# Performance work log

Measured on AMD Instinct MI355X. Metric: run time of the kernel, lower is better.

The kernel has to match this reference:

```python
import jax, jax.numpy as jnp
import numpy as np

EPS = 1e-5  # config.layer_norm_epsilon

def setup_inputs() -> dict:
    key = jax.random.key(0)
    ks = jax.random.split(key, 8)
    B, S, D, BOT, N = 8, 2048, 1024, 400, 25
    x = jax.random.normal(ks[0], (B, S, D), dtype=jnp.float32)
    alphas = jax.random.uniform(ks[1], (N,), dtype=jnp.float32) / N
    W_down_all = jax.random.normal(ks[2], (N, BOT, D), dtype=jnp.float32) * 0.02
    W_up_all = jax.random.normal(ks[3], (N, D, BOT), dtype=jnp.float32) * 0.02
    b_down_all = jax.random.normal(ks[4], (N, BOT), dtype=jnp.float32) * 0.02
    b_up_all = jax.random.normal(ks[5], (N, D), dtype=jnp.float32) * 0.02
    W_ln_all = 1.0 + jax.random.normal(ks[6], (N, D), dtype=jnp.float32) * 0.02
    b_ln_all = jax.random.normal(ks[7], (N, D), dtype=jnp.float32) * 0.02
    return {"x": x, "alphas": alphas, "W_down_all": W_down_all, "W_up_all": W_up_all,
            "b_down_all": b_down_all, "b_up_all": b_up_all,
            "W_ln_all": W_ln_all, "b_ln_all": b_ln_all}

def reference(x, alphas, W_down_all, W_up_all, b_down_all, b_up_all, W_ln_all, b_ln_all):
    # Superposition: alpha-weighted sum of all adapters' parameters
    # (original python loop over 25 adapters -> single einsum per tensor).
    W_down = jnp.einsum('n,nbd->bd', alphas, W_down_all)  # [BOT, D]
    W_up   = jnp.einsum('n,ndb->db', alphas, W_up_all)    # [D, BOT]
    W_ln   = jnp.einsum('n,nd->d',  alphas, W_ln_all)     # [D]
    b_ln   = jnp.einsum('n,nd->d',  alphas, b_ln_all)     # [D]
    # b_up / b_down are merged in the original too but passed with bias=None: unused.

    # FAdapter: F.layer_norm with normalized_shape = x.shape[1:], i.e. normalize
    # jointly over (seq, embd) per batch element; ln weight/bias broadcast over seq.
    mu = jnp.mean(x, axis=(1, 2), keepdims=True)
    var = jnp.mean(jnp.square(x - mu), axis=(1, 2), keepdims=True)
    x_ = (x - mu) * jax.lax.rsqrt(var + EPS) * W_ln + b_ln  # [B,S,D]

    h = jax.nn.relu(jnp.einsum('bsd,od->bso', x_, W_down))  # [B,S,BOT], no bias
    x_ = jnp.einsum('bso,do->bsd', h, W_up)                 # [B,S,D],   no bias
    return x + x_
```

## Files before the change

kernel.cpp:

```cpp
#include <hip/hip_runtime.h>
#include <stdint.h>

#define NB   8
#define SS   2048
#define DD   1024
#define BOT  400
#define BOTP 512
#define NAD  25
#define MM   (NB*SS)
#define LN_EPS 1e-5f

typedef __attribute__((ext_vector_type(8))) short bf8_t;
typedef __attribute__((ext_vector_type(4))) float fx4;

__device__ __forceinline__ unsigned short f2bf(float f) {
  unsigned int u = __float_as_uint(f);
  u = (u + 0x7FFFu + ((u >> 16) & 1u)) >> 16;
  return (unsigned short)u;
}

__device__ __forceinline__ void gload16(void* lds, const void* g) {
  __builtin_amdgcn_global_load_lds(
      (const __attribute__((address_space(1))) void*)(uintptr_t)g,
      (__attribute__((address_space(3))) void*)(uint32_t)(uintptr_t)lds,
      16, 0, 0);
}

__global__ __launch_bounds__(256) void mix_kernel(
    const float* __restrict__ alphas,
    const float* __restrict__ WdAll, const float* __restrict__ WuAll,
    const float* __restrict__ wlnAll, const float* __restrict__ blnAll,
    unsigned short* __restrict__ Wd, unsigned short* __restrict__ Wu,
    float* __restrict__ wln, float* __restrict__ bln)
{
  __shared__ float a[NAD];
  const int tid = threadIdx.x;
  if (tid < NAD) a[tid] = alphas[tid];
  __syncthreads();
  const int bid = blockIdx.x;
  if (bid < 512) {
    int g  = bid * 256 + tid;
    int o  = g >> 8;
    int dg = g & 255;
    float4 acc = {0.f, 0.f, 0.f, 0.f};
    if (o < BOT) {
#pragma unroll
      for (int n = 0; n < NAD; ++n) {
        const float4 v = *(const float4*)(WdAll + ((size_t)n * BOT + o) * DD + dg * 4);
        acc.x += a[n] * v.x; acc.y += a[n] * v.y; acc.z += a[n] * v.z; acc.w += a[n] * v.w;
      }
    }
    ushort4 u;
    u.x = f2bf(acc.x); u.y = f2bf(acc.y); u.z = f2bf(acc.z); u.w = f2bf(acc.w);
    *(ushort4*)(Wd + (size_t)o * DD + dg * 4) = u;
  } else if (bid < 1024) {
    int g  = (bid - 512) * 256 + tid;
    int d  = g >> 7;
    int bg = g & 127;
    float4 acc = {0.f, 0.f, 0.f, 0.f};
    if (bg < 100) {
#pragma unroll
      for (int n = 0; n < NAD; ++n) {
        const float4 v = *(const float4*)(WuAll + ((size_t)n * DD + d) * BOT + bg * 4);
        acc.x += a[n] * v.x; acc.y += a[n] * v.y; acc.z += a[n] * v.z; acc.w += a[n] * v.w;
      }
    }
    ushort4 u;
    u.x = f2bf(acc.x); u.y = f2bf(acc.y); u.z = f2bf(acc.z); u.w = f2bf(acc.w);
    *(ushort4*)(Wu + (size_t)d * BOTP + bg * 4) = u;
  } else {
    int i = (bid - 1024) * 256 + tid;
    const float* src = (i < DD) ? wlnAll : blnAll;
    int j = (i < DD) ? i : (i - DD);
    float s = 0.f;
#pragma unroll
    for (int n = 0; n < NAD; ++n) s += a[n] * src[(size_t)n * DD + j];
    if (i < DD) wln[j] = s; else bln[j] = s;
  }
}

__global__ __launch_bounds__(256) void stats_kernel(const float* __restrict__ x,
                                                    float* __restrict__ partials)
{
  const int b = blockIdx.y, c = blockIdx.x;
  const float4* xb = (const float4*)(x + (size_t)b * SS * DD) + (size_t)c * 8192;
  float s = 0.f, q = 0.f;
  for (int i = threadIdx.x; i < 8192; i += 256) {
    float4 v = xb[i];
    s += v.x + v.y + v.z + v.w;
    q += v.x * v.x + v.y * v.y + v.z * v.z + v.w * v.w;
  }
#pragma unroll
  for (int off = 32; off > 0; off >>= 1) { s += __shfl_down(s, off); q += __shfl_down(q, off); }
  __shared__ float red[8];
  const int wave = threadIdx.x >> 6, lane = threadIdx.x & 63;
  if (!lane) { red[wave] = s; red[wave + 4] = q; }
  __syncthreads();
  if (!threadIdx.x) {
    partials[(b * 64 + c) * 2]     = red[0] + red[1] + red[2] + red[3];
    partials[(b * 64 + c) * 2 + 1] = red[4] + red[5] + red[6] + red[7];
  }
}

__global__ __launch_bounds__(256) void norm_kernel(const float* __restrict__ x,
    const float* __restrict__ partials, const float* __restrict__ wln,
    const float* __restrict__ bln, unsigned short* __restrict__ xn)
{
  const int b = blockIdx.y;
  double s = 0.0, q = 0.0;
#pragma unroll 8
  for (int i = 0; i < 64; ++i) {
    s += partials[(b * 64 + i) * 2];
    q += partials[(b * 64 + i) * 2 + 1];
  }
  const double inv = 1.0 / ((double)SS * DD);
  const float mu  = (float)(s * inv);
  const float var = (float)(q * inv) - mu * mu;
  const float rs  = rsqrtf(var + LN_EPS);

  const size_t base = (size_t)b * SS * DD;
  const int idx = blockIdx.x * 256 + threadIdx.x;
  const float4 v  = *(const float4*)(x + base + (size_t)idx * 4);
  const int dg = idx & 255;
  const float4 w  = *(const float4*)(wln + dg * 4);
  const float4 bb = *(const float4*)(bln + dg * 4);
  ushort4 u;
  u.x = f2bf((v.x - mu) * rs * w.x + bb.x);
  u.y = f2bf((v.y - mu) * rs * w.y + bb.y);
  u.z = f2bf((v.z - mu) * rs * w.z + bb.z);
  u.w = f2bf((v.w - mu) * rs * w.w + bb.w);
  *(ushort4*)(xn + base + (size_t)idx * 4) = u;
}

template <int K, bool RELU>
__global__ __launch_bounds__(256) void gemm_bt(
    const unsigned short* __restrict__ A, const unsigned short* __restrict__ Bm,
    const float* __restrict__ Xres, float* __restrict__ Cf,
    unsigned short* __restrict__ Cb, int N)
{
  __shared__ unsigned short As[128 * 32];
  __shared__ unsigned short Bs[128 * 32];
  const int tid  = threadIdx.x;
  const int wave = tid >> 6, lane = tid & 63;
  const int wr = wave >> 1, wc = wave & 1;
  const int nbn  = N >> 7;
  const int bcol = blockIdx.x % nbn, brow = blockIdx.x / nbn;
  const unsigned short* Ab = A + (size_t)brow * 128 * K;
  const unsigned short* Bb = Bm + (size_t)bcol * 128 * K;

  fx4 acc[4][4] = {};

  for (int k0 = 0; k0 < K; k0 += 32) {
#pragma unroll
    for (int i = 0; i < 2; ++i) {
      const int basee = (i * 256 + wave * 64) * 8;
      const int e   = basee + lane * 8;
      const int row = e >> 5, col = e & 31;
      gload16(&As[basee], Ab + (size_t)row * K + k0 + col);
      gload16(&Bs[basee], Bb + (size_t)row * K + k0 + col);
    }
    __syncthreads();

    bf8_t af[4], bf[4];
#pragma unroll
    for (int m = 0; m < 4; ++m)
      af[m] = *(const bf8_t*)&As[(wr * 64 + m * 16 + (lane & 15)) * 32 + (lane >> 4) * 8];
#pragma unroll
    for (int n = 0; n < 4; ++n)
      bf[n] = *(const bf8_t*)&Bs[(wc * 64 + n * 16 + (lane & 15)) * 32 + (lane >> 4) * 8];
#pragma unroll
    for (int m = 0; m < 4; ++m)
#pragma unroll
      for (int n = 0; n < 4; ++n)
        acc[m][n] = __builtin_amdgcn_mfma_f32_16x16x32_bf16(af[m], bf[n], acc[m][n], 0, 0, 0);
    __syncthreads();
  }

  const int r0 = brow * 128 + wr * 64 + ((lane >> 4) << 2);
  const int c0 = bcol * 128 + wc * 64 + (lane & 15);
#pragma unroll
  for (int m = 0; m < 4; ++m) {
#pragma unroll
    for (int n = 0; n < 4; ++n) {
#pragma unroll
      for (int j = 0; j < 4; ++j) {
        const size_t off = (size_t)(r0 + m * 16 + j) * N + (c0 + n * 16);
        float v = acc[m][n][j];
        if (RELU) {
          v = v > 0.f ? v : 0.f;
          Cb[off] = f2bf(v);
        } else {
          Cf[off] = v + Xres[off];
        }
      }
    }
  }
}

extern "C" void kernel_launch(void* const* d_in, const int* in_sizes, int n_in,
                              void* d_out, int out_size, void* d_ws, size_t ws_size,
                              hipStream_t stream)
{
  const float* x      = (const float*)d_in[0];
  const float* alphas = (const float*)d_in[1];
  const float* WdAll  = (const float*)d_in[2];
  const float* WuAll  = (const float*)d_in[3];
  const float* wlnAll = (const float*)d_in[6];
  const float* blnAll = (const float*)d_in[7];
  float* out = (float*)d_out;

  char* ws = (char*)d_ws;
  unsigned short* Wd  = (unsigned short*)ws;
  unsigned short* Wu  = (unsigned short*)(ws + (1u << 20));
  float* wln          = (float*)(ws + (2u << 20));
  float* bln          = wln + DD;
  float* partials     = bln + DD;
  unsigned short* xn  = (unsigned short*)(ws + (3u << 20));
  unsigned short* h   = (unsigned short*)(ws + (35u << 20));

  mix_kernel<<<1032, 256, 0, stream>>>(alphas, WdAll, WuAll, wlnAll, blnAll, Wd, Wu, wln, bln);
  stats_kernel<<<dim3(64, 8), 256, 0, stream>>>(x, partials);
  norm_kernel<<<dim3(2048, 8), 256, 0, stream>>>(x, partials, wln, bln, xn);
  gemm_bt<1024, true ><<<128 * (BOTP / 128), 256, 0, stream>>>(xn, Wd, nullptr, nullptr, h, BOTP);
  gemm_bt<512,  false><<<128 * (DD / 128),   256, 0, stream>>>(h, Wu, x, out, nullptr, DD);
}
```

Baseline: 291.3 us.

## Double-buffer GEMM LDS tiles, swizzle block order, merge mix and stats kernels

Merges the weight-mixing and layer-norm statistics kernels into one launch, so the two independent jobs share a grid and one launch is saved. The GEMM now double-buffers its LDS tiles so the next k-tile loads while MFMAs run on the current one, and the first GEMM uses a 64-wide k-step. Block indices are remapped in an XCD-aware way (blockIdx & 7) to improve L2 locality. The ReLU GEMM stages its bf16 output through LDS to write coalesced 16-byte stores. Doubling the LDS footprint may reduce occupancy.

```diff
diff --git a/kernel.cpp b/kernel.cpp
--- a/kernel.cpp
+++ b/kernel.cpp
@@ -7,7 +7,6 @@
 #define BOT  400
 #define BOTP 512
 #define NAD  25
-#define MM   (NB*SS)
 #define LN_EPS 1e-5f
 
 typedef __attribute__((ext_vector_type(8))) short bf8_t;
@@ -26,18 +25,45 @@
       16, 0, 0);
 }
 
-__global__ __launch_bounds__(256) void mix_kernel(
+__global__ __launch_bounds__(256) void mixstats_kernel(
     const float* __restrict__ alphas,
     const float* __restrict__ WdAll, const float* __restrict__ WuAll,
     const float* __restrict__ wlnAll, const float* __restrict__ blnAll,
+    const float* __restrict__ x,
     unsigned short* __restrict__ Wd, unsigned short* __restrict__ Wu,
-    float* __restrict__ wln, float* __restrict__ bln)
-{
+    float* __restrict__ wln, float* __restrict__ bln,
+    float* __restrict__ partials)
+{
+  const int tid = threadIdx.x;
+  const int bid = blockIdx.x;
+
+  if (bid >= 1032) {
+    const int g = bid - 1032;
+    const int b = g >> 6, c = g & 63;
+    const float4* xb = (const float4*)(x + (size_t)b * SS * DD) + (size_t)c * 8192;
+    float s = 0.f, q = 0.f;
+    for (int i = tid; i < 8192; i += 256) {
+      float4 v = xb[i];
+      s += v.x + v.y + v.z + v.w;
+      q += v.x * v.x + v.y * v.y + v.z * v.z + v.w * v.w;
+    }
+#pragma unroll
+    for (int off = 32; off > 0; off >>= 1) { s += __shfl_down(s, off); q += __shfl_down(q, off); }
+    __shared__ float red[8];
+    const int wave = tid >> 6, lane = tid & 63;
+    if (!lane) { red[wave] = s; red[wave + 4] = q; }
+    __syncthreads();
+    if (!tid) {
+      partials[(b * 64 + c) * 2]     = red[0] + red[1] + red[2] + red[3];
+      partials[(b * 64 + c) * 2 + 1] = red[4] + red[5] + red[6] + red[7];
+    }
+    return;
+  }
+
   __shared__ float a[NAD];
-  const int tid = threadIdx.x;
   if (tid < NAD) a[tid] = alphas[tid];
   __syncthreads();
-  const int bid = blockIdx.x;
+
   if (bid < 512) {
     int g  = bid * 256 + tid;
     int o  = g >> 8;
@@ -76,29 +102,6 @@
 #pragma unroll
     for (int n = 0; n < NAD; ++n) s += a[n] * src[(size_t)n * DD + j];
     if (i < DD) wln[j] = s; else bln[j] = s;
-  }
-}
-
-__global__ __launch_bounds__(256) void stats_kernel(const float* __restrict__ x,
-                                                    float* __restrict__ partials)
-{
-  const int b = blockIdx.y, c = blockIdx.x;
-  const float4* xb = (const float4*)(x + (size_t)b * SS * DD) + (size_t)c * 8192;
-  float s = 0.f, q = 0.f;
-  for (int i = threadIdx.x; i < 8192; i += 256) {
-    float4 v = xb[i];
-    s += v.x + v.y + v.z + v.w;
-    q += v.x * v.x + v.y * v.y + v.z * v.z + v.w * v.w;
-  }
-#pragma unroll
-  for (int off = 32; off > 0; off >>= 1) { s += __shfl_down(s, off); q += __shfl_down(q, off); }
-  __shared__ float red[8];
-  const int wave = threadIdx.x >> 6, lane = threadIdx.x & 63;
-  if (!lane) { red[wave] = s; red[wave + 4] = q; }
-  __syncthreads();
-  if (!threadIdx.x) {
-    partials[(b * 64 + c) * 2]     = red[0] + red[1] + red[2] + red[3];
-    partials[(b * 64 + c) * 2 + 1] = red[4] + red[5] + red[6] + red[7];
   }
 }
 
@@ -132,68 +135,97 @@
   *(ushort4*)(xn + base + (size_t)idx * 4) = u;
 }
 
-template <int K, bool RELU>
+template <int K, int BK, bool RELU>
 __global__ __launch_bounds__(256) void gemm_bt(
     const unsigned short* __restrict__ A, const unsigned short* __restrict__ Bm,
     const float* __restrict__ Xres, float* __restrict__ Cf,
-    unsigned short* __restrict__ Cb, int N)
-{
-  __shared__ unsigned short As[128 * 32];
-  __shared__ unsigned short Bs[128 * 32];
+    unsigned short* __restrict__ Cb, int N, int nbn)
+{
+  __shared__ unsigned short As[2][128 * BK];
+  __shared__ unsigned short Bs[2][128 * BK];
   const int tid  = threadIdx.x;
   const int wave = tid >> 6, lane = tid & 63;
   const int wr = wave >> 1, wc = wave & 1;
-  const int nbn  = N >> 7;
-  const int bcol = blockIdx.x % nbn, brow = blockIdx.x / nbn;
+
+  const int cpx = gridDim.x >> 3;
+  const int bid = (blockIdx.x & 7) * cpx + (blockIdx.x >> 3);
+  const int bcol = bid % nbn, brow = bid / nbn;
   const unsigned short* Ab = A + (size_t)brow * 128 * K;
   const unsigned short* Bb = Bm + (size_t)bcol * 128 * K;
 
-  fx4 acc[4][4] = {};
-
-  for (int k0 = 0; k0 < K; k0 += 32) {
-#pragma unroll
-    for (int i = 0; i < 2; ++i) {
+  constexpr int NL = (128 * BK) / 2048;
+  auto stage = [&](int buf, int k0) {
+#pragma unroll
+    for (int i = 0; i < NL; ++i) {
       const int basee = (i * 256 + wave * 64) * 8;
       const int e   = basee + lane * 8;
-      const int row = e >> 5, col = e & 31;
-      gload16(&As[basee], Ab + (size_t)row * K + k0 + col);
-      gload16(&Bs[basee], Bb + (size_t)row * K + k0 + col);
+      const int row = e / BK, col = e % BK;
+      gload16(&As[buf][basee], Ab + (size_t)row * K + k0 + col);
+      gload16(&Bs[buf][basee], Bb + (size_t)row * K + k0 + col);
+    }
+  };
+
+  fx4 acc[4][4] = {};
+  constexpr int NT = K / BK;
+
+  stage(0, 0);
+  __syncthreads();
+  int cur = 0;
+  for (int t = 0; t < NT; ++t) {
+    if (t + 1 < NT) stage(cur ^ 1, (t + 1) * BK);
+#pragma unroll
+    for (int kk = 0; kk < BK / 32; ++kk) {
+      bf8_t af[4], bf[4];
+#pragma unroll
+      for (int m = 0; m < 4; ++m)
+        af[m] = *(const bf8_t*)&As[cur][(wr * 64 + m * 16 + (lane & 15)) * BK + kk * 32 + (lane >> 4) * 8];
+#pragma unroll
+      for (int n = 0; n < 4; ++n)
+        bf[n] = *(const bf8_t*)&Bs[cur][(wc * 64 + n * 16 + (lane & 15)) * BK + kk * 32 + (lane >> 4) * 8];
+#pragma unroll
+      for (int m = 0; m < 4; ++m)
+#pragma unroll
+        for (int n = 0; n < 4; ++n)
+          acc[m][n] = __builtin_amdgcn_mfma_f32_16x16x32_bf16(af[m], bf[n], acc[m][n], 0, 0, 0);
     }
     __syncthreads();
-
-    bf8_t af[4], bf[4];
+    cur ^= 1;
+  }
+
+  if constexpr (RELU) {
+    unsigned short* Hs = (unsigned short*)As;
+    const int r0l = wr * 64 + ((lane >> 4) << 2);
+    const int c0l = wc * 64 + (lane & 15);
 #pragma unroll
     for (int m = 0; m < 4; ++m)
-      af[m] = *(const bf8_t*)&As[(wr * 64 + m * 16 + (lane & 15)) * 32 + (lane >> 4) * 8];
-#pragma unroll
-    for (int n = 0; n < 4; ++n)
-      bf[n] = *(const bf8_t*)&Bs[(wc * 64 + n * 16 + (lane & 15)) * 32 + (lane >> 4) * 8];
+#pragma unroll
+      for (int n = 0; n < 4; ++n)
+#pragma unroll
+        for (int j = 0; j < 4; ++j) {
+          float v = acc[m][n][j];
+          v = v > 0.f ? v : 0.f;
+          Hs[(r0l + m * 16 + j) * 128 + (c0l + n * 16)] = f2bf(v);
+        }
+    __syncthreads();
+    const size_t outbase = (size_t)(brow * 128) * N + (size_t)bcol * 128;
+#pragma unroll
+    for (int i = 0; i < 8; ++i) {
+      const int idx = i * 256 + tid;
+      const int row = idx >> 4, colg = idx & 15;
+      *(int4*)(Cb + outbase + (size_t)row * N + colg * 8) = *(const int4*)&Hs[row * 128 + colg * 8];
+    }
+  } else {
+    const int r0 = brow * 128 + wr * 64 + ((lane >> 4) << 2);
+    const int c0 = bcol * 128 + wc * 64 + (lane & 15);
 #pragma unroll
     for (int m = 0; m < 4; ++m)
 #pragma unroll
       for (int n = 0; n < 4; ++n)
-        acc[m][n] = __builtin_amdgcn_mfma_f32_16x16x32_bf16(af[m], bf[n], acc[m][n], 0, 0, 0);
-    __syncthreads();
-  }
-
-  const int r0 = brow * 128 + wr * 64 + ((lane >> 4) << 2);
-  const int c0 = bcol * 128 + wc * 64 + (lane & 15);
-#pragma unroll
-  for (int m = 0; m < 4; ++m) {
-#pragma unroll
-    for (int n = 0; n < 4; ++n) {
-#pragma unroll
-      for (int j = 0; j < 4; ++j) {
-        const size_t off = (size_t)(r0 + m * 16 + j) * N + (c0 + n * 16);
-        float v = acc[m][n][j];
-        if (RELU) {
-          v = v > 0.f ? v : 0.f;
-          Cb[off] = f2bf(v);
-        } else {
-          Cf[off] = v + Xres[off];
+#pragma unroll
+        for (int j = 0; j < 4; ++j) {
+          const size_t off = (size_t)(r0 + m * 16 + j) * N + (c0 + n * 16);
+          Cf[off] = acc[m][n][j] + Xres[off];
         }
-      }
-    }
   }
 }
 
@@ -218,9 +250,9 @@
   unsigned short* xn  = (unsigned short*)(ws + (3u << 20));
   unsigned short* h   = (unsigned short*)(ws + (35u << 20));
 
-  mix_kernel<<<1032, 256, 0, stream>>>(alphas, WdAll, WuAll, wlnAll, blnAll, Wd, Wu, wln, bln);
-  stats_kernel<<<dim3(64, 8), 256, 0, stream>>>(x, partials);
+  mixstats_kernel<<<1544, 256, 0, stream>>>(alphas, WdAll, WuAll, wlnAll, blnAll, x,
+                                            Wd, Wu, wln, bln, partials);
   norm_kernel<<<dim3(2048, 8), 256, 0, stream>>>(x, partials, wln, bln, xn);
-  gemm_bt<1024, true ><<<128 * (BOTP / 128), 256, 0, stream>>>(xn, Wd, nullptr, nullptr, h, BOTP);
-  gemm_bt<512,  false><<<128 * (DD / 128),   256, 0, stream>>>(h, Wu, x, out, nullptr, DD);
-}
+  gemm_bt<1024, 64, true ><<<512,  256, 0, stream>>>(xn, Wd, nullptr, nullptr, h, BOTP, BOTP / 128);
+  gemm_bt<512,  32, false><<<1024, 256, 0, stream>>>(h, Wu, x, out, nullptr, DD, DD / 128);
+}
```

Result: slower. 301.5 us (+3.5%).

## Fuse layernorm into first GEMM, double-buffer both GEMMs, rework weight mixing

Applied to the files above, without the earlier changes.

The separate normalize kernel and its bf16 intermediate buffer are removed. The first GEMM now reads fp32 x directly, applies the folded scale and shift while converting to bf16 in LDS, and uses 64-wide K tiles with swizzling and double buffering. The second GEMM also gains double-buffered, swizzled LDS staging. The mix kernel is rewritten with flat indexing, loads hoisted into registers, packed bf16 conversion and explicit zeroing of the padding regions, and the stats kernel uses more chunks. Reading fp32 A costs more bandwidth and registers per tile than reading bf16 A.

```diff
diff --git a/kernel.cpp b/kernel.cpp
--- a/kernel.cpp
+++ b/kernel.cpp
@@ -7,8 +7,8 @@
 #define BOT  400
 #define BOTP 512
 #define NAD  25
-#define MM   (NB*SS)
 #define LN_EPS 1e-5f
+#define NCH  128
 
 typedef __attribute__((ext_vector_type(8))) short bf8_t;
 typedef __attribute__((ext_vector_type(4))) float fx4;
@@ -17,6 +17,11 @@
   unsigned int u = __float_as_uint(f);
   u = (u + 0x7FFFu + ((u >> 16) & 1u)) >> 16;
   return (unsigned short)u;
+}
+__device__ __forceinline__ uint32_t cvtpk(float lo, float hi) {
+  uint32_t r;
+  asm("v_cvt_pk_bf16_f32 %0, %1, %2" : "=v"(r) : "v"(lo), "v"(hi));
+  return r;
 }
 
 __device__ __forceinline__ void gload16(void* lds, const void* g) {
@@ -38,44 +43,46 @@
   if (tid < NAD) a[tid] = alphas[tid];
   __syncthreads();
   const int bid = blockIdx.x;
-  if (bid < 512) {
-    int g  = bid * 256 + tid;
-    int o  = g >> 8;
-    int dg = g & 255;
+
+  if (bid < 800) {
+    const int g = (bid < 400 ? bid : bid - 400) * 256 + tid;
+    const float4* src = (const float4*)(bid < 400 ? WdAll : WuAll) + g;
+    float4 vals[NAD];
+#pragma unroll
+    for (int n = 0; n < NAD; ++n) vals[n] = src[(size_t)n * 102400];
     float4 acc = {0.f, 0.f, 0.f, 0.f};
-    if (o < BOT) {
-#pragma unroll
-      for (int n = 0; n < NAD; ++n) {
-        const float4 v = *(const float4*)(WdAll + ((size_t)n * BOT + o) * DD + dg * 4);
-        acc.x += a[n] * v.x; acc.y += a[n] * v.y; acc.z += a[n] * v.z; acc.w += a[n] * v.w;
-      }
-    }
-    ushort4 u;
-    u.x = f2bf(acc.x); u.y = f2bf(acc.y); u.z = f2bf(acc.z); u.w = f2bf(acc.w);
-    *(ushort4*)(Wd + (size_t)o * DD + dg * 4) = u;
-  } else if (bid < 1024) {
-    int g  = (bid - 512) * 256 + tid;
-    int d  = g >> 7;
-    int bg = g & 127;
-    float4 acc = {0.f, 0.f, 0.f, 0.f};
-    if (bg < 100) {
-#pragma unroll
-      for (int n = 0; n < NAD; ++n) {
-        const float4 v = *(const float4*)(WuAll + ((size_t)n * DD + d) * BOT + bg * 4);
-        acc.x += a[n] * v.x; acc.y += a[n] * v.y; acc.z += a[n] * v.z; acc.w += a[n] * v.w;
-      }
-    }
-    ushort4 u;
-    u.x = f2bf(acc.x); u.y = f2bf(acc.y); u.z = f2bf(acc.z); u.w = f2bf(acc.w);
-    *(ushort4*)(Wu + (size_t)d * BOTP + bg * 4) = u;
+#pragma unroll
+    for (int n = 0; n < NAD; ++n) {
+      acc.x += a[n] * vals[n].x; acc.y += a[n] * vals[n].y;
+      acc.z += a[n] * vals[n].z; acc.w += a[n] * vals[n].w;
+    }
+    uint2 pk = { cvtpk(acc.x, acc.y), cvtpk(acc.z, acc.w) };
+    if (bid < 400) {
+      *(uint2*)(Wd + (size_t)g * 4) = pk;
+    } else {
+      const int d = g / 100, bg = g - d * 100;
+      *(uint2*)(Wu + (size_t)d * BOTP + bg * 4) = pk;
+    }
+  } else if (bid < 808) {
+    const int i = (bid - 800) * 256 + tid;
+    const float* src = (i < DD) ? wlnAll : blnAll;
+    const int j = (i < DD) ? i : (i - DD);
+    float v[NAD];
+#pragma unroll
+    for (int n = 0; n < NAD; ++n) v[n] = src[(size_t)n * DD + j];
+    float s = 0.f;
+#pragma unroll
+    for (int n = 0; n < NAD; ++n) s += a[n] * v[n];
+    if (i < DD) wln[j] = s; else bln[j] = s;
+  } else if (bid < 864) {
+    const int t = (bid - 808) * 256 + tid;
+    int4 z = {0, 0, 0, 0};
+    *(int4*)(Wd + 400 * 1024 + (size_t)t * 8) = z;
   } else {
-    int i = (bid - 1024) * 256 + tid;
-    const float* src = (i < DD) ? wlnAll : blnAll;
-    int j = (i < DD) ? i : (i - DD);
-    float s = 0.f;
-#pragma unroll
-    for (int n = 0; n < NAD; ++n) s += a[n] * src[(size_t)n * DD + j];
-    if (i < DD) wln[j] = s; else bln[j] = s;
+    const int t = (bid - 864) * 256 + tid;
+    const int row = t / 14, c8 = t - row * 14;
+    int4 z = {0, 0, 0, 0};
+    *(int4*)(Wu + (size_t)row * BOTP + 400 + c8 * 8) = z;
   }
 }
 
@@ -83,9 +90,10 @@
                                                     float* __restrict__ partials)
 {
   const int b = blockIdx.y, c = blockIdx.x;
-  const float4* xb = (const float4*)(x + (size_t)b * SS * DD) + (size_t)c * 8192;
+  const float4* xb = (const float4*)(x + (size_t)b * SS * DD) + (size_t)c * 4096;
   float s = 0.f, q = 0.f;
-  for (int i = threadIdx.x; i < 8192; i += 256) {
+#pragma unroll 4
+  for (int i = threadIdx.x; i < 4096; i += 256) {
     float4 v = xb[i];
     s += v.x + v.y + v.z + v.w;
     q += v.x * v.x + v.y * v.y + v.z * v.z + v.w * v.w;
@@ -97,77 +105,193 @@
   if (!lane) { red[wave] = s; red[wave + 4] = q; }
   __syncthreads();
   if (!threadIdx.x) {
-    partials[(b * 64 + c) * 2]     = red[0] + red[1] + red[2] + red[3];
-    partials[(b * 64 + c) * 2 + 1] = red[4] + red[5] + red[6] + red[7];
-  }
-}
-
-__global__ __launch_bounds__(256) void norm_kernel(const float* __restrict__ x,
+    partials[(b * NCH + c) * 2]     = red[0] + red[1] + red[2] + red[3];
+    partials[(b * NCH + c) * 2 + 1] = red[4] + red[5] + red[6] + red[7];
+  }
+}
+
+__global__ __launch_bounds__(256) void gemm1(
+    const float* __restrict__ x, const unsigned short* __restrict__ Bw,
     const float* __restrict__ partials, const float* __restrict__ wln,
-    const float* __restrict__ bln, unsigned short* __restrict__ xn)
-{
-  const int b = blockIdx.y;
-  double s = 0.0, q = 0.0;
+    const float* __restrict__ bln, unsigned short* __restrict__ H)
+{
+  __shared__ unsigned short As[2][128 * 64];
+  __shared__ unsigned short Bs[2][128 * 64];
+  __shared__ float s1[DD], s2[DD];
+  const int tid = threadIdx.x, wave = tid >> 6, lane = tid & 63;
+  const int wr = wave >> 1, wc = wave & 1;
+  const int bid = (blockIdx.x & 7) * 64 + (blockIdx.x >> 3);
+  const int bcol = bid & 3, brow = bid >> 2;
+  const int b = brow >> 4;
+
+  double sd = 0.0, qd = 0.0;
 #pragma unroll 8
-  for (int i = 0; i < 64; ++i) {
-    s += partials[(b * 64 + i) * 2];
-    q += partials[(b * 64 + i) * 2 + 1];
-  }
-  const double inv = 1.0 / ((double)SS * DD);
-  const float mu  = (float)(s * inv);
-  const float var = (float)(q * inv) - mu * mu;
+  for (int i = 0; i < NCH; ++i) {
+    sd += partials[(b * NCH + i) * 2];
+    qd += partials[(b * NCH + i) * 2 + 1];
+  }
+  const float mu  = (float)(sd * (1.0 / 2097152.0));
+  const float var = (float)(qd * (1.0 / 2097152.0)) - mu * mu;
   const float rs  = rsqrtf(var + LN_EPS);
-
-  const size_t base = (size_t)b * SS * DD;
-  const int idx = blockIdx.x * 256 + threadIdx.x;
-  const float4 v  = *(const float4*)(x + base + (size_t)idx * 4);
-  const int dg = idx & 255;
-  const float4 w  = *(const float4*)(wln + dg * 4);
-  const float4 bb = *(const float4*)(bln + dg * 4);
-  ushort4 u;
-  u.x = f2bf((v.x - mu) * rs * w.x + bb.x);
-  u.y = f2bf((v.y - mu) * rs * w.y + bb.y);
-  u.z = f2bf((v.z - mu) * rs * w.z + bb.z);
-  u.w = f2bf((v.w - mu) * rs * w.w + bb.w);
-  *(ushort4*)(xn + base + (size_t)idx * 4) = u;
-}
-
-template <int K, bool RELU>
-__global__ __launch_bounds__(256) void gemm_bt(
+  for (int c = tid; c < DD; c += 256) {
+    const float v1 = rs * wln[c];
+    s1[c] = v1; s2[c] = bln[c] - mu * v1;
+  }
+
+  const float* Ab = x + (size_t)(brow * 128) * DD;
+  const unsigned short* Bb = Bw + (size_t)(bcol * 128) * DD;
+  const int arow = tid >> 3;
+  const int c8   = tid & 7;
+  const int aswz = (arow & 7) << 4;
+
+  auto loadA = [&](int k0, float4* xr) {
+#pragma unroll
+    for (int i = 0; i < 4; ++i) {
+      const float* p = Ab + (size_t)(i * 32 + arow) * DD + k0 + c8 * 8;
+      xr[i * 2]     = *(const float4*)p;
+      xr[i * 2 + 1] = *(const float4*)(p + 4);
+    }
+  };
+  auto writeA = [&](int buf, int k0, const float4* xr) {
+    const float4 w0 = *(const float4*)&s1[k0 + c8 * 8];
+    const float4 w1 = *(const float4*)&s1[k0 + c8 * 8 + 4];
+    const float4 b0 = *(const float4*)&s2[k0 + c8 * 8];
+    const float4 b1 = *(const float4*)&s2[k0 + c8 * 8 + 4];
+#pragma unroll
+    for (int i = 0; i < 4; ++i) {
+      const float4 v0 = xr[i * 2], v1 = xr[i * 2 + 1];
+      uint4 pk;
+      pk.x = cvtpk(v0.x * w0.x + b0.x, v0.y * w0.y + b0.y);
+      pk.y = cvtpk(v0.z * w0.z + b0.z, v0.w * w0.w + b0.w);
+      pk.z = cvtpk(v1.x * w1.x + b1.x, v1.y * w1.y + b1.y);
+      pk.w = cvtpk(v1.z * w1.z + b1.z, v1.w * w1.w + b1.w);
+      *(uint4*)((char*)&As[buf][0] + (i * 32 + arow) * 128 + ((c8 * 16) ^ aswz)) = pk;
+    }
+  };
+  auto stageB = [&](int buf, int k0) {
+#pragma unroll
+    for (int i = 0; i < 4; ++i) {
+      const int q   = i * 256 + wave * 64;
+      const int ql  = q + lane;
+      const int row = ql >> 3, c16 = ql & 7;
+      const int o   = c16 ^ (row & 7);
+      gload16(&Bs[buf][q * 8], Bb + (size_t)row * DD + k0 + o * 8);
+    }
+  };
+
+  fx4 acc[4][4] = {};
+  auto compute = [&](int buf) {
+#pragma unroll
+    for (int kk = 0; kk < 2; ++kk) {
+      bf8_t af[4], bf[4];
+#pragma unroll
+      for (int m = 0; m < 4; ++m) {
+        const int r = wr * 64 + m * 16 + (lane & 15);
+        af[m] = *(const bf8_t*)((const char*)&As[buf][0] + r * 128 +
+                                ((kk * 64 + (lane >> 4) * 16) ^ ((r & 7) << 4)));
+      }
+#pragma unroll
+      for (int n = 0; n < 4; ++n) {
+        const int r = wc * 64 + n * 16 + (lane & 15);
+        bf[n] = *(const bf8_t*)((const char*)&Bs[buf][0] + r * 128 +
+                                ((kk * 64 + (lane >> 4) * 16) ^ ((r & 7) << 4)));
+      }
+#pragma unroll
+      for (int m = 0; m < 4; ++m)
+#pragma unroll
+        for (int n = 0; n < 4; ++n)
+          acc[m][n] = __builtin_amdgcn_mfma_f32_16x16x32_bf16(af[m], bf[n], acc[m][n], 0, 0, 0);
+    }
+  };
+
+  float4 xrA[8], xrB[8];
+  loadA(0, xrA); stageB(0, 0);
+  __syncthreads();
+  writeA(0, 0, xrA);
+  __syncthreads();
+#pragma unroll 1
+  for (int t2 = 0; t2 < 8; ++t2) {
+    {
+      const int t = t2 * 2;
+      if (t < 15) { loadA((t + 1) * 64, xrB); stageB(1, (t + 1) * 64); }
+      compute(0);
+      if (t < 15) writeA(1, (t + 1) * 64, xrB);
+      __syncthreads();
+    }
+    {
+      const int t = t2 * 2 + 1;
+      if (t < 15) { loadA((t + 1) * 64, xrA); stageB(0, (t + 1) * 64); }
+      compute(1);
+      if (t < 15) writeA(0, (t + 1) * 64, xrA);
+      __syncthreads();
+    }
+  }
+
+  unsigned short* Hs = &As[0][0];
+  const int r0l = wr * 64 + ((lane >> 4) << 2);
+  const int c0l = wc * 64 + (lane & 15);
+#pragma unroll
+  for (int m = 0; m < 4; ++m)
+#pragma unroll
+    for (int n = 0; n < 4; ++n)
+#pragma unroll
+      for (int j = 0; j < 4; ++j) {
+        float v = acc[m][n][j];
+        Hs[(r0l + m * 16 + j) * 128 + (c0l + n * 16)] = f2bf(v > 0.f ? v : 0.f);
+      }
+  __syncthreads();
+  const size_t outbase = (size_t)(brow * 128) * BOTP + (size_t)bcol * 128;
+#pragma unroll
+  for (int i = 0; i < 8; ++i) {
+    const int idx = i * 256 + tid;
+    const int row = idx >> 4, colg = idx & 15;
+    *(int4*)(H + outbase + (size_t)row * BOTP + colg * 8) = *(const int4*)&Hs[row * 128 + colg * 8];
+  }
+}
+
+__global__ __launch_bounds__(256) void gemm2(
     const unsigned short* __restrict__ A, const unsigned short* __restrict__ Bm,
-    const float* __restrict__ Xres, float* __restrict__ Cf,
-    unsigned short* __restrict__ Cb, int N)
-{
-  __shared__ unsigned short As[128 * 32];
-  __shared__ unsigned short Bs[128 * 32];
-  const int tid  = threadIdx.x;
-  const int wave = tid >> 6, lane = tid & 63;
+    const float* __restrict__ Xres, float* __restrict__ out)
+{
+  __shared__ unsigned short As[2][128 * 32];
+  __shared__ unsigned short Bs[2][128 * 32];
+  const int tid = threadIdx.x, wave = tid >> 6, lane = tid & 63;
   const int wr = wave >> 1, wc = wave & 1;
-  const int nbn  = N >> 7;
-  const int bcol = blockIdx.x % nbn, brow = blockIdx.x / nbn;
-  const unsigned short* Ab = A + (size_t)brow * 128 * K;
-  const unsigned short* Bb = Bm + (size_t)bcol * 128 * K;
+  const int bid = (blockIdx.x & 7) * 128 + (blockIdx.x >> 3);
+  const int bcol = bid & 7, brow = bid >> 3;
+  const unsigned short* Ab = A + (size_t)(brow * 128) * BOTP;
+  const unsigned short* Bb = Bm + (size_t)(bcol * 128) * BOTP;
+
+  auto stage = [&](int buf, int k0) {
+#pragma unroll
+    for (int i = 0; i < 2; ++i) {
+      const int q   = i * 256 + wave * 64;
+      const int ql  = q + lane;
+      const int row = ql >> 2, c16 = ql & 3;
+      const int o   = c16 ^ (row & 3);
+      gload16(&As[buf][q * 8], Ab + (size_t)row * BOTP + k0 + o * 8);
+      gload16(&Bs[buf][q * 8], Bb + (size_t)row * BOTP + k0 + o * 8);
+    }
+  };
 
   fx4 acc[4][4] = {};
-
-  for (int k0 = 0; k0 < K; k0 += 32) {
-#pragma unroll
-    for (int i = 0; i < 2; ++i) {
-      const int basee = (i * 256 + wave * 64) * 8;
-      const int e   = basee + lane * 8;
-      const int row = e >> 5, col = e & 31;
-      gload16(&As[basee], Ab + (size_t)row * K + k0 + col);
-      gload16(&Bs[basee], Bb + (size_t)row * K + k0 + col);
-    }
-    __syncthreads();
-
+  stage(0, 0);
+  __syncthreads();
+  for (int t = 0; t < 16; ++t) {
+    const int cur = t & 1;
+    if (t < 15) stage(cur ^ 1, (t + 1) * 32);
     bf8_t af[4], bf[4];
-#pragma unroll
-    for (int m = 0; m < 4; ++m)
-      af[m] = *(const bf8_t*)&As[(wr * 64 + m * 16 + (lane & 15)) * 32 + (lane >> 4) * 8];
-#pragma unroll
-    for (int n = 0; n < 4; ++n)
-      bf[n] = *(const bf8_t*)&Bs[(wc * 64 + n * 16 + (lane & 15)) * 32 + (lane >> 4) * 8];
+    const int hi16 = (lane >> 4) * 16;
+#pragma unroll
+    for (int m = 0; m < 4; ++m) {
+      const int r = wr * 64 + m * 16 + (lane & 15);
+      af[m] = *(const bf8_t*)((const char*)&As[cur][0] + r * 64 + (hi16 ^ ((r & 3) << 4)));
+    }
+#pragma unroll
+    for (int n = 0; n < 4; ++n) {
+      const int r = wc * 64 + n * 16 + (lane & 15);
+      bf[n] = *(const bf8_t*)((const char*)&Bs[cur][0] + r * 64 + (hi16 ^ ((r & 3) << 4)));
+    }
 #pragma unroll
     for (int m = 0; m < 4; ++m)
 #pragma unroll
@@ -179,22 +303,14 @@
   const int r0 = brow * 128 + wr * 64 + ((lane >> 4) << 2);
   const int c0 = bcol * 128 + wc * 64 + (lane & 15);
 #pragma unroll
-  for (int m = 0; m < 4; ++m) {
-#pragma unroll
-    for (int n = 0; n < 4; ++n) {
+  for (int m = 0; m < 4; ++m)
+#pragma unroll
+    for (int n = 0; n < 4; ++n)
 #pragma unroll
       for (int j = 0; j < 4; ++j) {
-        const size_t off = (size_t)(r0 + m * 16 + j) * N + (c0 + n * 16);
-        float v = acc[m][n][j];
-        if (RELU) {
-          v = v > 0.f ? v : 0.f;
-          Cb[off] = f2bf(v);
-        } else {
-          Cf[off] = v + Xres[off];
-        }
+        const size_t off = (size_t)(r0 + m * 16 + j) * DD + (c0 + n * 16);
+        out[off] = acc[m][n][j] + Xres[off];
       }
-    }
-  }
 }
 
 extern "C" void kernel_launch(void* const* d_in, const int* in_sizes, int n_in,
@@ -215,12 +331,10 @@
   float* wln          = (float*)(ws + (2u << 20));
   float* bln          = wln + DD;
   float* partials     = bln + DD;
-  unsigned short* xn  = (unsigned short*)(ws + (3u << 20));
-  unsigned short* h   = (unsigned short*)(ws + (35u << 20));
-
-  mix_kernel<<<1032, 256, 0, stream>>>(alphas, WdAll, WuAll, wlnAll, blnAll, Wd, Wu, wln, bln);
-  stats_kernel<<<dim3(64, 8), 256, 0, stream>>>(x, partials);
-  norm_kernel<<<dim3(2048, 8), 256, 0, stream>>>(x, partials, wln, bln, xn);
-  gemm_bt<1024, true ><<<128 * (BOTP / 128), 256, 0, stream>>>(xn, Wd, nullptr, nullptr, h, BOTP);
-  gemm_bt<512,  false><<<128 * (DD / 128),   256, 0, stream>>>(h, Wu, x, out, nullptr, DD);
-}
+  unsigned short* h   = (unsigned short*)(ws + (3u << 20));
+
+  mix_kernel<<<920, 256, 0, stream>>>(alphas, WdAll, WuAll, wlnAll, blnAll, Wd, Wu, wln, bln);
+  stats_kernel<<<dim3(NCH, NB), 256, 0, stream>>>(x, partials);
+  gemm1<<<512, 256, 0, stream>>>(x, Wd, partials, wln, bln, h);
+  gemm2<<<1024, 256, 0, stream>>>(h, Wu, x, out);
+}
```

New measurement: 274.7 us. 1.06x faster.
